# Performance work log

Measured on AMD Instinct MI355X. Metric: run time of the kernel, lower is better.

The kernel has to match this reference:

```python
import jax, jax.numpy as jnp
import numpy as np
from jax import lax
from jax.scipy.special import logsumexp

B, T, K, D = 16, 128, 1024, 768
APPROX_R = 0.1
LAMBD = 0.1
KP = int(APPROX_R * K)  # num_state_approx = 102


def setup_inputs() -> dict:
    key = jax.random.key(0)
    k0, k1, k2, k3 = jax.random.split(key, 4)
    x_emb = jax.random.normal(k0, (B, T, D), jnp.float32)
    # nn.Parameter(torch.normal(0, norm_scale_transition, [K, D]))
    state_matrix = 0.01 * jax.random.normal(k1, (K, D), jnp.float32)
    y = jax.random.randint(k2, (B, T), 0, K)
    y_lens = jax.random.randint(k3, (B,), 1, T + 1)
    return {"x_emb": x_emb, "state_matrix": state_matrix, "y": y, "y_lens": y_lens}


def _forward_sum(transition, emission, y_lens):
    # exact linear-chain CRF forward (logsumexp) scan. emission: [B,T,K]
    bsz = emission.shape[0]
    def step(alpha, em_t):
        new = logsumexp(alpha[:, :, None] + transition[None], axis=1) + em_t
        return new, new
    a0 = emission[:, 0]
    _, rest = lax.scan(step, a0, jnp.swapaxes(emission, 0, 1)[1:])
    alphas = jnp.concatenate([a0[None], rest], axis=0)  # [T,B,K]
    a_last = alphas[y_lens - 1, jnp.arange(bsz)]        # [B,K]
    return logsumexp(a_last, axis=-1)


def _approx_forward(state_matrix, emission, y_lens, kp):
    # restricted forward over the top-kp states (by emission potential) per
    # position; transitions among selected states computed on the fly from
    # state embeddings (avoids the full KxK transition).
    bsz = emission.shape[0]
    d = state_matrix.shape[1]
    em_top, idx = lax.top_k(emission, kp)   # [B,T,KP]
    st_sel = state_matrix[idx]              # [B,T,KP,D]
    def step(carry, inp):
        alpha, st_prev = carry
        em_t, st_t = inp
        trans_t = jnp.einsum('bid,bjd->bij', st_prev, st_t) / np.sqrt(d)
        new = logsumexp(alpha[:, :, None] + trans_t, axis=1) + em_t
        return (new, st_t), new
    a0 = em_top[:, 0]
    xs = (jnp.swapaxes(em_top, 0, 1)[1:], jnp.swapaxes(st_sel, 0, 1)[1:])
    _, rest = lax.scan(step, (a0, st_sel[:, 0]), xs)
    alphas = jnp.concatenate([a0[None], rest], axis=0)
    a_last = alphas[y_lens - 1, jnp.arange(bsz)]
    return logsumexp(a_last, axis=-1)


def _viterbi(transition, emission, y_lens):
    bsz, tlen, k = emission.shape
    def step(alpha, em_t):
        scores = alpha[:, :, None] + transition[None]
        bp = jnp.argmax(scores, axis=1).astype(jnp.int32)
        new = jnp.max(scores, axis=1) + em_t
        return new, (new, bp)
    a0 = emission[:, 0]
    _, (rest, bps) = lax.scan(step, a0, jnp.swapaxes(emission, 0, 1)[1:])
    alphas = jnp.concatenate([a0[None], rest], axis=0)  # [T,B,K]
    a_last = alphas[y_lens - 1, jnp.arange(bsz)]
    last_state = jnp.argmax(a_last, axis=-1).astype(jnp.int32)
    # bps[t] maps best state at t+1 -> state at t; pad to length T
    bps_pad = jnp.concatenate([bps, jnp.zeros((1, bsz, k), jnp.int32)], axis=0)
    def back(s, inp):
        t, bp_t = inp
        cand = jnp.take_along_axis(bp_t, s[:, None], axis=1)[:, 0]
        s_new = jnp.where(t == y_lens - 1, last_state,
                          jnp.where(t < y_lens - 1, cand, 0))
        return s_new, s_new
    ts = jnp.arange(tlen)[::-1]
    _, s_seq = lax.scan(back, jnp.zeros((bsz,), jnp.int32), (ts, bps_pad[::-1]))
    return jnp.swapaxes(s_seq[::-1], 0, 1)  # [B,T]


def _evaluate(y_pred, y, y_lens, mask_f):
    support = ((y > 0).astype(jnp.float32) * mask_f).sum()
    pred = ((y_pred > 0).astype(jnp.float32) * mask_f).sum()
    overlap = (((y_pred > 0) & (y > 0)).astype(jnp.float32) * mask_f).sum()
    acc = ((y_pred == y).astype(jnp.float32) * mask_f).sum() / y_lens.sum()
    prec = jnp.where(pred > 0, overlap / jnp.maximum(pred, 1.0), 0.0)
    recl = overlap / jnp.maximum(support, 1.0)
    f1 = jnp.where(prec > 0, 2 * prec * recl / jnp.maximum(prec + recl, 1e-12), 0.0)
    return acc, prec, recl, f1


def reference(x_emb, state_matrix, y, y_lens):
    d = x_emb.shape[-1]
    bsz, tlen = y.shape
    emission = jnp.einsum('btd,kd->btk', x_emb, state_matrix) / np.sqrt(d)
    transition = jnp.matmul(state_matrix, state_matrix.T) / np.sqrt(d)

    log_Z = _forward_sum(transition, emission, y_lens)
    log_Z_approx = _approx_forward(state_matrix, emission, y_lens, KP)

    # gold sequence log potential, masked by lengths
    pos = jnp.arange(tlen)
    mask = (pos[None, :] < y_lens[:, None])
    mask_f = mask.astype(jnp.float32)
    mask_tr = (pos[None, :tlen - 1] < (y_lens - 1)[:, None]).astype(jnp.float32)
    em_y = jnp.take_along_axis(emission, y[..., None], axis=-1)[..., 0]
    trans_y = transition[y[:, :-1], y[:, 1:]]
    log_y_potential = (em_y * mask_f).sum(-1) + (trans_y * mask_tr).sum(-1)

    seq_log_prob_exact = -(log_y_potential - log_Z).mean()
    seq_log_prob_approx = -(log_y_potential - log_Z_approx).mean()

    total_len = y_lens.sum()
    logp = jax.nn.log_softmax(emission, axis=-1)
    lp_y = jnp.take_along_axis(logp, y[..., None], axis=-1)[..., 0]
    seq_log_prob_local = (lp_y * mask_f).sum() / total_len
    max_prob = (jnp.max(jax.nn.softmax(emission, -1), -1) * mask_f).sum() / total_len

    # loss_type == 'approx_crf'
    loss = seq_log_prob_approx + LAMBD * seq_log_prob_local

    crf_output = _viterbi(transition, emission, y_lens)
    crf_acc, crf_prec, crf_recl, crf_f1 = _evaluate(crf_output, y, y_lens, mask_f)
    softmax_output = emission.argmax(-1)
    sm_acc, sm_prec, sm_recl, sm_f1 = _evaluate(softmax_output, y, y_lens, mask_f)

    return (loss, crf_output, log_Z.mean(), log_Z_approx.mean(),
            seq_log_prob_exact, seq_log_prob_local, max_prob,
            crf_acc, crf_f1, sm_acc, sm_f1)


if __name__ == '__main__':
    out = reference(**setup_inputs())
    print(out[0], out[2], out[3])
```

## Files before the change

kernel.cpp:

```cpp
#include <hip/hip_runtime.h>
#include <cstdint>
#include <cstddef>

typedef unsigned long long ull;
typedef unsigned int uint32;
typedef unsigned short u16;
typedef __attribute__((ext_vector_type(8))) short s8v;
typedef __attribute__((ext_vector_type(4))) float f32x4;


#define POISON32 0xFFFFFFFFu
#define POISON64 0xFFFFFFFFFFFFFFFFull

#define OFF_EM    ((size_t)0)
#define OFF_TR    ((size_t)2097152)
#define OFF_EXPTB ((size_t)3145728)
#define OFF_UPP   ((size_t)3670016)
#define OFF_APP   ((size_t)3735552)
#define OFF_ULST  ((size_t)3801088)
#define OFF_ALST  ((size_t)3817472)
#define OFF_UALST ((size_t)3833856)
#define OFF_ETOP  ((size_t)3835904)
#define OFF_ITOP  ((size_t)4044800)
#define OFF_RMAX  ((size_t)4253696)
#define OFF_RLSE  ((size_t)4255744)
#define OFF_SMP   ((size_t)4257792)
#define OFF_BP    ((size_t)4259840)
#define OFF_DONE  ((size_t)6356992)
#define OFF_EXPTT ((size_t)6367744)

__device__ __forceinline__ u16 f2bf(float f) {
  uint32 u = __builtin_bit_cast(uint32, f);
  u = (u + 0x7fffu + ((u >> 16) & 1u)) >> 16;
  return (u16)u;
}
__device__ __forceinline__ float bflo(uint32 w) {
  return __builtin_bit_cast(float, w << 16);
}
__device__ __forceinline__ float bfhi(uint32 w) {
  return __builtin_bit_cast(float, w & 0xffff0000u);
}
__device__ __forceinline__ void bfsplit(float v, u16& h, u16& l) {
  h = f2bf(v);
  float rh = __builtin_bit_cast(float, ((uint32)h) << 16);
  l = f2bf(v - rh);
}

__device__ __forceinline__ ull load_bypass_u64(const ull* p) {
  return __hip_atomic_load(p, __ATOMIC_RELAXED, __HIP_MEMORY_SCOPE_AGENT);
}
__device__ __forceinline__ void store_bypass_u64(ull* p, ull v) {
  __hip_atomic_store(p, v, __ATOMIC_RELAXED, __HIP_MEMORY_SCOPE_AGENT);
}
__device__ __forceinline__ uint32 load_bypass_u32(const uint32* p) {
  return __hip_atomic_load(p, __ATOMIC_RELAXED, __HIP_MEMORY_SCOPE_AGENT);
}
__device__ __forceinline__ void store_bypass_u32(uint32* p, uint32 v) {
  __hip_atomic_store(p, v, __ATOMIC_RELAXED, __HIP_MEMORY_SCOPE_AGENT);
}
__device__ __forceinline__ void store_bypass_u16(u16* p, u16 v) {
  __hip_atomic_store(p, v, __ATOMIC_RELAXED, __HIP_MEMORY_SCOPE_AGENT);
}
__device__ __forceinline__ float load_bypass_f(const float* p) {
  return __hip_atomic_load(p, __ATOMIC_RELAXED, __HIP_MEMORY_SCOPE_AGENT);
}
__device__ __forceinline__ void store_bypass_f(float* p, float v) {
  __hip_atomic_store(p, v, __ATOMIC_RELAXED, __HIP_MEMORY_SCOPE_AGENT);
}
__device__ __forceinline__ void store_bypass_i(int* p, int v) {
  __hip_atomic_store(p, v, __ATOMIC_RELAXED, __HIP_MEMORY_SCOPE_AGENT);
}
__device__ __forceinline__ int load_bypass_i(const int* p) {
  return __hip_atomic_load(p, __ATOMIC_RELAXED, __HIP_MEMORY_SCOPE_AGENT);
}

__global__ __launch_bounds__(256) void gemm_kernel(
    const float* __restrict__ x, const float* __restrict__ stm,
    float* __restrict__ emission, float* __restrict__ transition,
    u16* __restrict__ expTb) {
  __shared__ float As[16][68];
  __shared__ float Bs[16][68];
  const int tid = threadIdx.x;
  const int tx = tid & 15, ty = tid >> 4;
  const int m0 = blockIdx.x * 64, n0 = blockIdx.y * 64;
  const int lr = tid >> 2;
  const int lc = (tid & 3) << 2;
  float acc[4][4] = {};
  const float* aptr;
  {
    int gr = m0 + lr;
    aptr = (gr < 2048) ? (x + (size_t)gr * 768) : (stm + (size_t)(gr - 2048) * 768);
  }
  const float* bptr = stm + (size_t)(n0 + lr) * 768;
  for (int k0 = 0; k0 < 768; k0 += 16) {
    float4 a4 = *(const float4*)(aptr + k0 + lc);
    float4 b4 = *(const float4*)(bptr + k0 + lc);
    __syncthreads();
    As[lc + 0][lr] = a4.x; As[lc + 1][lr] = a4.y; As[lc + 2][lr] = a4.z; As[lc + 3][lr] = a4.w;
    Bs[lc + 0][lr] = b4.x; Bs[lc + 1][lr] = b4.y; Bs[lc + 2][lr] = b4.z; Bs[lc + 3][lr] = b4.w;
    __syncthreads();
#pragma unroll
    for (int kk = 0; kk < 16; ++kk) {
      float a[4], b[4];
#pragma unroll
      for (int q = 0; q < 4; ++q) a[q] = As[kk][ty * 4 + q];
#pragma unroll
      for (int q = 0; q < 4; ++q) b[q] = Bs[kk][tx * 4 + q];
#pragma unroll
      for (int i2 = 0; i2 < 4; ++i2)
#pragma unroll
        for (int j2 = 0; j2 < 4; ++j2) acc[i2][j2] += a[i2] * b[j2];
    }
  }
  const float rs = 0.03608439182435161f;
#pragma unroll
  for (int i2 = 0; i2 < 4; ++i2) {
    int r = m0 + ty * 4 + i2;
#pragma unroll
    for (int j2 = 0; j2 < 4; ++j2) {
      int c = n0 + tx * 4 + j2;
      float v = acc[i2][j2] * rs;
      if (r < 2048) {
        emission[(size_t)r * 1024 + c] = v;
      } else {
        size_t o = (size_t)(r - 2048) * 1024 + c;
        transition[o] = v;
        expTb[o] = f2bf(expf(v));
      }
    }
  }
}

__global__ __launch_bounds__(256) void transT_kernel(
    const u16* __restrict__ src, u16* __restrict__ dst) {
  __shared__ u16 tile[64][65];
  const int bx = blockIdx.x * 64, by = blockIdx.y * 64;
  const int tx = threadIdx.x & 63, ty4 = threadIdx.x >> 6;
  for (int rr = ty4; rr < 64; rr += 4)
    tile[rr][tx] = src[(size_t)(bx + rr) * 1024 + by + tx];
  __syncthreads();
  for (int rr = ty4; rr < 64; rr += 4)
    dst[(size_t)(by + rr) * 1024 + bx + tx] = tile[tx][rr];
}

__global__ __launch_bounds__(256) void topk_kernel(
    const float* __restrict__ emission, float* __restrict__ em_top,
    int* __restrict__ top_idx, float* __restrict__ row_max,
    float* __restrict__ row_lse, int* __restrict__ sm_pred) {
  __shared__ float v[1024];
  __shared__ int ix[1024];
  __shared__ float rb[256];
  const int row = blockIdx.x;
  const int tid = threadIdx.x;
  const float* e = emission + (size_t)row * 1024;
  for (int p = tid; p < 1024; p += 256) { v[p] = e[p]; ix[p] = p; }
  __syncthreads();
  for (int k = 2; k <= 1024; k <<= 1) {
    for (int j = k >> 1; j > 0; j >>= 1) {
      for (int p = tid; p < 1024; p += 256) {
        int l = p ^ j;
        if (l > p) {
          float va = v[p], vb = v[l];
          int ia = ix[p], ib = ix[l];
          bool aBefore = (va > vb) || (va == vb && ia < ib);
          bool up = ((p & k) == 0);
          if (up ? !aBefore : aBefore) { v[p] = vb; v[l] = va; ix[p] = ib; ix[l] = ia; }
        }
      }
      __syncthreads();
    }
  }
  float mx = v[0];
  float s = 0.f;
  for (int p = tid; p < 1024; p += 256) s += expf(v[p] - mx);
  rb[tid] = s; __syncthreads();
  for (int w = 128; w > 0; w >>= 1) { if (tid < w) rb[tid] += rb[tid + w]; __syncthreads(); }
  if (tid == 0) {
    row_max[row] = mx;
    row_lse[row] = mx + logf(rb[0]);
    sm_pred[row] = ix[0];
  }
  for (int p = tid; p < 102; p += 256) {
    em_top[(size_t)row * 102 + p] = v[p];
    top_idx[(size_t)row * 102 + p] = ix[p];
  }
}

__global__ __launch_bounds__(256) void poison_kernel(ull* __restrict__ done8) {
  const int idx = blockIdx.x * 256 + threadIdx.x;
  store_bypass_u64(done8 + idx, POISON64);
}

__global__ __launch_bounds__(512) void scan_kernel(
    const float* __restrict__ em, const float* __restrict__ tr,
    const u16* __restrict__ expTb, const u16* __restrict__ expTbT,
    const float* __restrict__ em_top, const int* __restrict__ top_idx,
    const int* __restrict__ y_lens,
    float* __restrict__ u_ring, float* __restrict__ av_ring,
    float* __restrict__ u_last, float* __restrict__ av_last,
    float* __restrict__ ua_last, int* __restrict__ bp,
    uint32* __restrict__ done, float* __restrict__ out_crf) {
  __shared__ ull SH[9232];
  const int bid = blockIdx.x, tid = threadIdx.x;
  uint32* sentF = done;
  uint32* sentV = done + 512;
  uint32* vdone = done + 8704;

  if (bid < 8) {
    const int p = bid;
    int* stbF = (int*)(SH + 8192);
    if (tid < 16) stbF[tid] = y_lens[tid] - 1;
    const int l = tid & 63;
    const int lm = l & 15, lq = l >> 4;
    const int w2 = (tid >> 6) & 3;
    if (tid < 256) {
      const int m = tid >> 4;
      const int nn = p * 128 + ((tid & 15) << 3);
      const float* e0 = em + ((size_t)m << 17) + nn;
      u16* rh = (u16*)u_ring;
      const bool last0 = (y_lens[m] == 1);
#pragma unroll
      for (int q = 0; q < 8; ++q) {
        float v = expf(e0[q]);
        u16 h, lo2; bfsplit(v, h, lo2);
        store_bypass_u16(rh + m * 1024 + nn + q, h);
        store_bypass_u16(rh + 16384 + m * 1024 + nn + q, lo2);
        if (last0) u_last[(size_t)m * 1024 + nn + q] = v;
      }
    }
    __syncthreads();
    if (tid == 0) {
      asm volatile("s_waitcnt vmcnt(0)" ::: "memory");
      store_bypass_u32(sentF + p * 16, 0u);
    }
    const char* Ab = (const char*)SH;
    const int offh = (lm << 11) + (lq << 4);
    const int axor = (lm & 7) << 4;
    const int nbase = p * 128 + w2 * 32;
    const u16* bq0 = expTbT + ((size_t)(nbase + lm) << 10) + (lq << 3);
    const u16* bq1 = bq0 + (16 << 10);
    for (int t = 1; t < 128; ++t) {
      if (tid < 8) {
        const uint32* sp = sentF + (size_t)((t - 1) & 3) * 128 + tid * 16;
        while (load_bypass_u32(sp) == POISON32) __builtin_amdgcn_s_sleep(1);
      }
      __syncthreads();
      if (tid == 0)
        store_bypass_u32(sentF + (size_t)((t + 2) & 3) * 128 + p * 16, POISON32);
      {
        const ull* src = (const ull*)(u_ring + (size_t)((t - 1) & 3) * 16384);
        ull dbuf[16];
#pragma unroll
        for (int q = 0; q < 16; ++q) dbuf[q] = load_bypass_u64(src + tid + (q << 9));
#pragma unroll
        for (int q = 0; q < 16; ++q) {
          const int ob = (tid + (q << 9)) << 3;
          *(ull*)((char*)SH + (ob ^ (((ob >> 11) & 7) << 4))) = dbuf[q];
        }
      }
      __syncthreads();
      if (tid < 256) {
        f32x4 acc0a = {0.f, 0.f, 0.f, 0.f}, acc0b = {0.f, 0.f, 0.f, 0.f};
        f32x4 acc1a = {0.f, 0.f, 0.f, 0.f}, acc1b = {0.f, 0.f, 0.f, 0.f};
        for (int k0 = 0; k0 < 1024; k0 += 64) {
          const int o0 = (offh + (k0 << 1)) ^ axor;
          const int o1 = (offh + ((k0 + 32) << 1)) ^ axor;
          s8v ah0 = *(const s8v*)(Ab + o0);
          s8v al0 = *(const s8v*)(Ab + 32768 + o0);
          s8v ah1 = *(const s8v*)(Ab + o1);
          s8v al1 = *(const s8v*)(Ab + 32768 + o1);
          s8v b00 = *(const s8v*)(bq0 + k0);
          s8v b10 = *(const s8v*)(bq1 + k0);
          s8v b01 = *(const s8v*)(bq0 + k0 + 32);
          s8v b11 = *(const s8v*)(bq1 + k0 + 32);
          acc0a = __builtin_amdgcn_mfma_f32_16x16x32_bf16(ah0, b00, acc0a, 0, 0, 0);
          acc1a = __builtin_amdgcn_mfma_f32_16x16x32_bf16(ah0, b10, acc1a, 0, 0, 0);
          acc0b = __builtin_amdgcn_mfma_f32_16x16x32_bf16(ah1, b01, acc0b, 0, 0, 0);
          acc1b = __builtin_amdgcn_mfma_f32_16x16x32_bf16(ah1, b11, acc1b, 0, 0, 0);
          acc0a = __builtin_amdgcn_mfma_f32_16x16x32_bf16(al0, b00, acc0a, 0, 0, 0);
          acc1a = __builtin_amdgcn_mfma_f32_16x16x32_bf16(al0, b10, acc1a, 0, 0, 0);
          acc0b = __builtin_amdgcn_mfma_f32_16x16x32_bf16(al1, b01, acc0b, 0, 0, 0);
          acc1b = __builtin_amdgcn_mfma_f32_16x16x32_bf16(al1, b11, acc1b, 0, 0, 0);
        }
        u16* rh = (u16*)(u_ring + (size_t)(t & 3) * 16384);
        const float sc = 1.0f / 1024.0f;
#pragma unroll
        for (int r = 0; r < 4; ++r) {
          const int m = (lq << 2) + r;
          const size_t erow = (((size_t)m << 7) + t) << 10;
          {
            const int n = nbase + lm;
            float v = (acc0a[r] + acc0b[r]) * sc * expf(em[erow + n]);
            u16 h, lo2; bfsplit(v, h, lo2);
            store_bypass_u16(rh + m * 1024 + n, h);
            store_bypass_u16(rh + 16384 + m * 1024 + n, lo2);
            if (t == stbF[m]) u_last[(size_t)m * 1024 + n] = v;
          }
          {
            const int n = nbase + 16 + lm;
            float v = (acc1a[r] + acc1b[r]) * sc * expf(em[erow + n]);
            u16 h, lo2; bfsplit(v, h, lo2);
            store_bypass_u16(rh + m * 1024 + n, h);
            store_bypass_u16(rh + 16384 + m * 1024 + n, lo2);
            if (t == stbF[m]) u_last[(size_t)m * 1024 + n] = v;
          }
        }
        asm volatile("s_waitcnt vmcnt(0)" ::: "memory");
      }
      __syncthreads();
      if (tid == 0) store_bypass_u32(sentF + (size_t)(t & 3) * 128 + p * 16, 0u);
    }
  } else if (bid < 136) {
    const int v = bid - 8;
    const int n0v = ((v & 7) << 7) + ((v >> 3) << 3);
    const int jj = tid & 7, g = tid >> 3;
    const int col = n0v + jj;
    ull* ppb = (ull*)((char*)SH + 65536);
    int* stb2 = (int*)((char*)SH + 73728);
    if (tid < 16) stb2[tid] = y_lens[tid] - 1;
    if (tid < 128) {
      const int jb = tid & 7, b = tid >> 3;
      const float e0 = em[((size_t)b << 17) + n0v + jb];
      store_bypass_f(av_ring + (size_t)(n0v + jb) * 16 + b, e0);
      if (y_lens[b] == 1) store_bypass_f(av_last + ((size_t)b << 10) + n0v + jb, e0);
    }
    __syncthreads();
    if (tid == 0) {
      asm volatile("s_waitcnt vmcnt(0)" ::: "memory");
      store_bypass_u32(sentV + v * 16, 0u);
    }
    const char* stc = (const char*)SH;
    for (int t = 1; t < 128; ++t) {
      if (tid < 128) {
        const uint32* sp = sentV + (size_t)((t - 1) & 3) * 2048 + tid * 16;
        while (load_bypass_u32(sp) == POISON32) __builtin_amdgcn_s_sleep(1);
      }
      __syncthreads();
      if (tid == 0)
        store_bypass_u32(sentV + (size_t)((t + 2) & 3) * 2048 + v * 16, POISON32);
      {
        const ull* src = (const ull*)(av_ring + (size_t)((t - 1) & 3) * 16384);
        ull dbuf[16];
#pragma unroll
        for (int q = 0; q < 16; ++q) dbuf[q] = load_bypass_u64(src + tid + (q << 9));
#pragma unroll
        for (int q = 0; q < 16; ++q) {
          const int ob = (tid + (q << 9)) << 3;
          *(ull*)((char*)SH + (ob ^ (((ob >> 10) & 7) << 4))) = dbuf[q];
        }
      }
      __syncthreads();
      float mv[16]; int mi[16];
#pragma unroll
      for (int b = 0; b < 16; ++b) { mv[b] = -3.0e38f; mi[b] = 0x7fffffff; }
      const float* trc = tr + col;
      const int i0 = g << 4;
#pragma unroll 4
      for (int ii = 0; ii < 16; ++ii) {
        const int i = i0 + ii;
        const float tv = trc[(size_t)i << 10];
        const int ph = (i << 6) ^ (((i >> 4) & 7) << 4);
        const f32x4 s0 = *(const f32x4*)(stc + (ph ^ 0));
        const f32x4 s1 = *(const f32x4*)(stc + (ph ^ 16));
        const f32x4 s2 = *(const f32x4*)(stc + (ph ^ 32));
        const f32x4 s3 = *(const f32x4*)(stc + (ph ^ 48));
#pragma unroll
        for (int b = 0; b < 4; ++b) {
          float c0 = s0[b] + tv; if (c0 > mv[b])      { mv[b] = c0;      mi[b] = i; }
          float c1 = s1[b] + tv; if (c1 > mv[b + 4])  { mv[b + 4] = c1;  mi[b + 4] = i; }
          float c2 = s2[b] + tv; if (c2 > mv[b + 8])  { mv[b + 8] = c2;  mi[b + 8] = i; }
          float c3 = s3[b] + tv; if (c3 > mv[b + 12]) { mv[b + 12] = c3; mi[b + 12] = i; }
        }
      }
#pragma unroll
      for (int d = 8; d <= 32; d <<= 1) {
#pragma unroll
        for (int b = 0; b < 16; ++b) {
          float ov = __shfl_xor(mv[b], d);
          int oi = __shfl_xor(mi[b], d);
          if (ov > mv[b] || (ov == mv[b] && oi < mi[b])) { mv[b] = ov; mi[b] = oi; }
        }
      }
      if ((tid & 63) < 8) {
        const int wv = tid >> 6;
#pragma unroll
        for (int b = 0; b < 16; ++b) {
          ull pk = ((ull)(uint32)mi[b] << 32) | (ull)__builtin_bit_cast(uint32, mv[b]);
          ppb[(b << 6) + (wv << 3) + jj] = pk;
        }
      }
      __syncthreads();
      if (tid < 128) {
        const int jb = tid & 7, b = tid >> 3;
        const int cf = n0v + jb;
        float bmv = -3.0e38f; int bmi = 0x7fffffff;
#pragma unroll
        for (int w = 0; w < 8; ++w) {
          ull pk = ppb[(b << 6) + (w << 3) + jb];
          float pv = __builtin_bit_cast(float, (uint32)pk);
          int pi = (int)(pk >> 32);
          if (pv > bmv || (pv == bmv && pi < bmi)) { bmv = pv; bmi = pi; }
        }
        const float nv = bmv + em[((((size_t)b << 7) + t) << 10) + cf];
        store_bypass_f(av_ring + (size_t)(t & 3) * 16384 + (size_t)cf * 16 + b, nv);
        store_bypass_i(bp + ((size_t)t << 14) + ((size_t)b << 10) + cf, bmi);
        if (t == stb2[b]) store_bypass_f(av_last + ((size_t)b << 10) + cf, nv);
        asm volatile("s_waitcnt vmcnt(0)" ::: "memory");
      }
      __syncthreads();
      if (tid == 0) store_bypass_u32(sentV + (size_t)(t & 3) * 2048 + v * 16, 0u);
    }
    if (tid == 0) {
      asm volatile("s_waitcnt vmcnt(0)" ::: "memory");
      store_bypass_u32(vdone + v * 16, 0u);
    }
    if (v == 0) {
      if (tid < 128) {
        while (load_bypass_u32(vdone + tid * 16) == POISON32) __builtin_amdgcn_s_sleep(1);
      }
      __syncthreads();
      const int wv = tid >> 6, lh = tid & 63;
      const int hb = lh >> 5, hl = lh & 31;
      const int b = wv * 2 + hb;
      const int tbb = y_lens[b] - 1;
      for (int t2 = tbb + 1 + hl; t2 < 128; t2 += 32) out_crf[(b << 7) + t2] = 0.f;
      float bv = -3.0e38f; int bi = 0x7fffffff;
      for (int q = 0; q < 32; ++q) {
        const int i = (q << 5) + hl;
        const float val = load_bypass_f(av_last + ((size_t)b << 10) + i);
        if (val > bv || (val == bv && i < bi)) { bv = val; bi = i; }
      }
#pragma unroll
      for (int d = 1; d < 32; d <<= 1) {
        float ov = __shfl_xor(bv, d, 32);
        int oi = __shfl_xor(bi, d, 32);
        if (ov > bv || (ov == bv && oi < bi)) { bv = ov; bi = oi; }
      }
      if (hl == 0) {
        int sx = bi;
        out_crf[(b << 7) + tbb] = (float)sx;
        for (int t2 = tbb - 1; t2 >= 0; --t2) {
          sx = load_bypass_i(bp + ((size_t)(t2 + 1) << 14) + ((size_t)b << 10) + sx);
          out_crf[(b << 7) + t2] = (float)sx;
        }
      }
    }
  } else {
    const int b = bid - 136;
    const int tb = y_lens[b] - 1;
    const int j2 = tid & 127, h2 = tid >> 7;
    float* sua0 = (float*)SH;
    float* sua1 = sua0 + 104;
    int* sidxp = (int*)(sua0 + 208);
    int* sidxc = sidxp + 104;
    float* aps = (float*)(sidxc + 104);
    if (tid < 102) {
      float vv = expf(em_top[(size_t)(b * 128) * 102 + tid]);
      sua0[tid] = vv;
      if (tb == 0) ua_last[b * 102 + tid] = vv;
    }
    __syncthreads();
    for (int t = 1; t < 128; ++t) {
      if (tid < 102) sidxp[tid] = top_idx[((size_t)b * 128 + (t - 1)) * 102 + tid];
      else if (tid >= 256 && tid < 358)
        sidxc[tid - 256] = top_idx[((size_t)b * 128 + t) * 102 + (tid - 256)];
      __syncthreads();
      float acc2 = 0.f;
      float* up = (t & 1) ? sua0 : sua1;
      float* cur = (t & 1) ? sua1 : sua0;
      if (j2 < 102) {
        const int colc = sidxc[j2];
        const int ia = h2 * 26;
        const int ib2 = (ia + 26 < 102) ? ia + 26 : 102;
        for (int i = ia; i < ib2; ++i)
          acc2 += up[i] * bflo((uint32)expTb[(size_t)sidxp[i] * 1024 + colc]);
      }
      if (h2 > 0 && j2 < 102) aps[(h2 - 1) * 104 + j2] = acc2;
      __syncthreads();
      if (h2 == 0 && j2 < 102) {
        acc2 += aps[j2] + aps[104 + j2] + aps[208 + j2];
        const float e = em_top[((size_t)b * 128 + t) * 102 + j2];
        const float nv = acc2 * expf(e) * (1.0f / 102.0f);
        cur[j2] = nv;
        if (t == tb) ua_last[b * 102 + j2] = nv;
      }
      __syncthreads();
    }
  }
}

__device__ __forceinline__ float blk_sum(float v, float* rb, int tid) {
  rb[tid] = v; __syncthreads();
  for (int w = 128; w > 0; w >>= 1) { if (tid < w) rb[tid] += rb[tid + w]; __syncthreads(); }
  float r = rb[0]; __syncthreads();
  return r;
}

__global__ __launch_bounds__(256) void finalize_kernel(
    const float* __restrict__ emission, const float* __restrict__ transition,
    const float* __restrict__ u_last, const float* __restrict__ ua_last,
    const float* __restrict__ row_max, const float* __restrict__ row_lse,
    const int* __restrict__ sm_pred, const int* __restrict__ y,
    const int* __restrict__ y_lens, float* __restrict__ d_out) {
  __shared__ float rb[256];
  __shared__ float sZ[16], sZa[16], sLogy[16];
  const int tid = threadIdx.x;
  const float* out_crf = d_out + 1;
  for (int b = 0; b < 16; ++b) {
    const int tb = y_lens[b] - 1;
    float p = 0.f;
    for (int i = tid; i < 1024; i += 256) p += u_last[(size_t)b * 1024 + i];
    p = blk_sum(p, rb, tid);
    if (tid == 0) sZ[b] = logf(p) + (float)tb * 6.931471805599453f;
    float q = 0.f;
    for (int i = tid; i < 102; i += 256) q += ua_last[(size_t)b * 102 + i];
    q = blk_sum(q, rb, tid);
    if (tid == 0) sZa[b] = logf(q) + (float)tb * 4.624972813284271f;
  }
  if (tid < 16) sLogy[tid] = 0.f;
  __syncthreads();
  float a_local = 0, a_maxp = 0, c_sup = 0, c_pred = 0, c_ov = 0, c_match = 0;
  float s_predc = 0, s_ov = 0, s_match = 0;
  for (int r = tid; r < 2048; r += 256) {
    const int b = r >> 7, t = r & 127;
    const int L = y_lens[b];
    if (t < L) {
      const int yv = y[r];
      const float em_y = emission[(size_t)r * 1024 + yv];
      const float lse = row_lse[r];
      a_local += em_y - lse;
      a_maxp += expf(row_max[r] - lse);
      float term = em_y;
      if (t < L - 1) term += transition[(size_t)yv * 1024 + y[r + 1]];
      atomicAdd(&sLogy[b], term);
      const float ypos = (yv > 0) ? 1.f : 0.f;
      c_sup += ypos;
      const int cs = (int)out_crf[r];
      c_pred += (cs > 0) ? 1.f : 0.f;
      c_ov += ((cs > 0) && (yv > 0)) ? 1.f : 0.f;
      c_match += (cs == yv) ? 1.f : 0.f;
      const int ss = sm_pred[r];
      s_predc += (ss > 0) ? 1.f : 0.f;
      s_ov += ((ss > 0) && (yv > 0)) ? 1.f : 0.f;
      s_match += (ss == yv) ? 1.f : 0.f;
    }
  }
  __syncthreads();
  a_local = blk_sum(a_local, rb, tid);
  a_maxp = blk_sum(a_maxp, rb, tid);
  c_sup = blk_sum(c_sup, rb, tid);
  c_pred = blk_sum(c_pred, rb, tid);
  c_ov = blk_sum(c_ov, rb, tid);
  c_match = blk_sum(c_match, rb, tid);
  s_predc = blk_sum(s_predc, rb, tid);
  s_ov = blk_sum(s_ov, rb, tid);
  s_match = blk_sum(s_match, rb, tid);
  if (tid == 0) {
    float tl = 0.f;
    for (int b = 0; b < 16; ++b) tl += (float)y_lens[b];
    float mZ = 0, mZa = 0, dE = 0, dA = 0;
    for (int b = 0; b < 16; ++b) {
      mZ += sZ[b]; mZa += sZa[b];
      dE += sLogy[b] - sZ[b];
      dA += sLogy[b] - sZa[b];
    }
    mZ *= (1.f / 16.f); mZa *= (1.f / 16.f);
    const float sle = -dE * (1.f / 16.f);
    const float sla = -dA * (1.f / 16.f);
    const float slocal = a_local / tl;
    const float maxp = a_maxp / tl;
    const float loss = sla + 0.1f * slocal;
    const float crf_acc = c_match / tl;
    const float crf_prec = (c_pred > 0.f) ? (c_ov / fmaxf(c_pred, 1.f)) : 0.f;
    const float crf_recl = c_ov / fmaxf(c_sup, 1.f);
    const float crf_f1 = (crf_prec > 0.f)
        ? (2.f * crf_prec * crf_recl / fmaxf(crf_prec + crf_recl, 1e-12f)) : 0.f;
    const float sm_acc = s_match / tl;
    const float sm_prec = (s_predc > 0.f) ? (s_ov / fmaxf(s_predc, 1.f)) : 0.f;
    const float sm_recl = s_ov / fmaxf(c_sup, 1.f);
    const float sm_f1 = (sm_prec > 0.f)
        ? (2.f * sm_prec * sm_recl / fmaxf(sm_prec + sm_recl, 1e-12f)) : 0.f;
    d_out[0] = loss;
    d_out[2049] = mZ;
    d_out[2050] = mZa;
    d_out[2051] = sle;
    d_out[2052] = slocal;
    d_out[2053] = maxp;
    d_out[2054] = crf_acc;
    d_out[2055] = crf_f1;
    d_out[2056] = sm_acc;
    d_out[2057] = sm_f1;
  }
}

extern "C" void kernel_launch(void* const* d_in, const int* in_sizes, int n_in,
                              void* d_out, int out_size, void* d_ws, size_t ws_size,
                              hipStream_t stream) {
  const float* x = (const float*)d_in[0];
  const float* stm = (const float*)d_in[1];
  const int* y = (const int*)d_in[2];
  const int* yl = (const int*)d_in[3];
  float* out = (float*)d_out;
  float* ws = (float*)d_ws;

  float* emission = ws + OFF_EM;
  float* transition = ws + OFF_TR;
  u16* expTb = (u16*)(ws + OFF_EXPTB);
  u16* expTbT = (u16*)(ws + OFF_EXPTT);
  float* u_ring = ws + OFF_UPP;
  float* av_ring = ws + OFF_APP;
  float* u_last = ws + OFF_ULST;
  float* av_last = ws + OFF_ALST;
  float* ua_last = ws + OFF_UALST;
  float* em_top = ws + OFF_ETOP;
  int* top_idx = (int*)(ws + OFF_ITOP);
  float* row_max = ws + OFF_RMAX;
  float* row_lse = ws + OFF_RLSE;
  int* sm_pred = (int*)(ws + OFF_SMP);
  int* bp = (int*)(ws + OFF_BP);
  uint32* done = (uint32*)(ws + OFF_DONE);

  poison_kernel<<<21, 256, 0, stream>>>((ull*)done);
  gemm_kernel<<<dim3(48, 16), 256, 0, stream>>>(x, stm, emission, transition, expTb);
  transT_kernel<<<dim3(16, 16), 256, 0, stream>>>(expTb, expTbT);
  topk_kernel<<<2048, 256, 0, stream>>>(emission, em_top, top_idx, row_max, row_lse, sm_pred);
  scan_kernel<<<152, 512, 0, stream>>>(emission, transition, expTb, expTbT, em_top, top_idx,
                                       yl, u_ring, av_ring, u_last, av_last, ua_last,
                                       bp, done, out + 1);
  finalize_kernel<<<1, 256, 0, stream>>>(emission, transition, u_last, ua_last,
                                         row_max, row_lse, sm_pred, y, yl, out);
}
```

Measured before the change: 1.914 ms.

## Replace per-block poison flags with atomic arrival counters in scan sync

Swaps the cross-block handshake in the persistent scan kernel. Each producer block used to write its own flag, and consumers polled many flags and re-poisoned slots in a 4-deep ring. Now producer blocks atomically increment a shared counter per ring slot (one counter per slot for the 8 forward blocks, and per slot and column group for the 128 Viterbi blocks), and a few threads poll it against a monotonically increasing target. The aim is to cut per-step polling traffic and the re-poison stores, at the cost of atomic contention on a handful of counters. The vmcnt wait moves to every writing thread before the barrier.

```diff
diff --git a/kernel.cpp b/kernel.cpp
--- a/kernel.cpp
+++ b/kernel.cpp
@@ -8,9 +8,6 @@
 typedef __attribute__((ext_vector_type(8))) short s8v;
 typedef __attribute__((ext_vector_type(4))) float f32x4;
 
-
-#define POISON32 0xFFFFFFFFu
-#define POISON64 0xFFFFFFFFFFFFFFFFull
 
 #define OFF_EM    ((size_t)0)
 #define OFF_TR    ((size_t)2097152)
@@ -72,6 +69,9 @@
 }
 __device__ __forceinline__ int load_bypass_i(const int* p) {
   return __hip_atomic_load(p, __ATOMIC_RELAXED, __HIP_MEMORY_SCOPE_AGENT);
+}
+__device__ __forceinline__ void cnt_add(uint32* p) {
+  __hip_atomic_fetch_add(p, 1u, __ATOMIC_RELAXED, __HIP_MEMORY_SCOPE_AGENT);
 }
 
 __global__ __launch_bounds__(256) void gemm_kernel(
@@ -186,9 +186,9 @@
   }
 }
 
-__global__ __launch_bounds__(256) void poison_kernel(ull* __restrict__ done8) {
+__global__ __launch_bounds__(256) void zero_kernel(uint32* __restrict__ done) {
   const int idx = blockIdx.x * 256 + threadIdx.x;
-  store_bypass_u64(done8 + idx, POISON64);
+  store_bypass_u32(done + idx, 0u);
 }
 
 __global__ __launch_bounds__(512) void scan_kernel(
@@ -202,9 +202,9 @@
     uint32* __restrict__ done, float* __restrict__ out_crf) {
   __shared__ ull SH[9232];
   const int bid = blockIdx.x, tid = threadIdx.x;
-  uint32* sentF = done;
-  uint32* sentV = done + 512;
-  uint32* vdone = done + 8704;
+  uint32* cntF = done;
+  uint32* cntV = done + 64;
+  uint32* vdone = done + 640;
 
   if (bid < 8) {
     const int p = bid;
@@ -227,12 +227,10 @@
         store_bypass_u16(rh + 16384 + m * 1024 + nn + q, lo2);
         if (last0) u_last[(size_t)m * 1024 + nn + q] = v;
       }
+      asm volatile("s_waitcnt vmcnt(0)" ::: "memory");
     }
     __syncthreads();
-    if (tid == 0) {
-      asm volatile("s_waitcnt vmcnt(0)" ::: "memory");
-      store_bypass_u32(sentF + p * 16, 0u);
-    }
+    if (tid == 0) cnt_add(cntF + 0);
     const char* Ab = (const char*)SH;
     const int offh = (lm << 11) + (lq << 4);
     const int axor = (lm & 7) << 4;
@@ -240,13 +238,12 @@
     const u16* bq0 = expTbT + ((size_t)(nbase + lm) << 10) + (lq << 3);
     const u16* bq1 = bq0 + (16 << 10);
     for (int t = 1; t < 128; ++t) {
-      if (tid < 8) {
-        const uint32* sp = sentF + (size_t)((t - 1) & 3) * 128 + tid * 16;
-        while (load_bypass_u32(sp) == POISON32) __builtin_amdgcn_s_sleep(1);
-      }
-      __syncthreads();
-      if (tid == 0)
-        store_bypass_u32(sentF + (size_t)((t + 2) & 3) * 128 + p * 16, POISON32);
+      if (tid == 0) {
+        const uint32 tgt = (uint32)((((t - 1) >> 2) + 1) * 8);
+        const uint32* cp = cntF + (((t - 1) & 3) << 4);
+        while (load_bypass_u32(cp) < tgt) __builtin_amdgcn_s_sleep(1);
+      }
+      __syncthreads();
       {
         const ull* src = (const ull*)(u_ring + (size_t)((t - 1) & 3) * 16384);
         ull dbuf[16];
@@ -308,7 +305,7 @@
         asm volatile("s_waitcnt vmcnt(0)" ::: "memory");
       }
       __syncthreads();
-      if (tid == 0) store_bypass_u32(sentF + (size_t)(t & 3) * 128 + p * 16, 0u);
+      if (tid == 0) cnt_add(cntF + ((t & 3) << 4));
     }
   } else if (bid < 136) {
     const int v = bid - 8;
@@ -323,21 +320,18 @@
       const float e0 = em[((size_t)b << 17) + n0v + jb];
       store_bypass_f(av_ring + (size_t)(n0v + jb) * 16 + b, e0);
       if (y_lens[b] == 1) store_bypass_f(av_last + ((size_t)b << 10) + n0v + jb, e0);
+      asm volatile("s_waitcnt vmcnt(0)" ::: "memory");
     }
     __syncthreads();
-    if (tid == 0) {
-      asm volatile("s_waitcnt vmcnt(0)" ::: "memory");
-      store_bypass_u32(sentV + v * 16, 0u);
-    }
+    if (tid == 0) cnt_add(cntV + ((v & 7) << 4));
     const char* stc = (const char*)SH;
     for (int t = 1; t < 128; ++t) {
-      if (tid < 128) {
-        const uint32* sp = sentV + (size_t)((t - 1) & 3) * 2048 + tid * 16;
-        while (load_bypass_u32(sp) == POISON32) __builtin_amdgcn_s_sleep(1);
-      }
-      __syncthreads();
-      if (tid == 0)
-        store_bypass_u32(sentV + (size_t)((t + 2) & 3) * 2048 + v * 16, POISON32);
+      if (tid < 8) {
+        const uint32 tgt = (uint32)((((t - 1) >> 2) + 1) * 16);
+        const uint32* cp = cntV + (((((t - 1) & 3) << 3) + tid) << 4);
+        while (load_bypass_u32(cp) < tgt) __builtin_amdgcn_s_sleep(1);
+      }
+      __syncthreads();
       {
         const ull* src = (const ull*)(av_ring + (size_t)((t - 1) & 3) * 16384);
         ull dbuf[16];
@@ -408,15 +402,12 @@
         asm volatile("s_waitcnt vmcnt(0)" ::: "memory");
       }
       __syncthreads();
-      if (tid == 0) store_bypass_u32(sentV + (size_t)(t & 3) * 2048 + v * 16, 0u);
-    }
-    if (tid == 0) {
-      asm volatile("s_waitcnt vmcnt(0)" ::: "memory");
-      store_bypass_u32(vdone + v * 16, 0u);
-    }
+      if (tid == 0) cnt_add(cntV + ((((t & 3) << 3) + (v & 7)) << 4));
+    }
+    if (tid == 0) cnt_add(vdone);
     if (v == 0) {
-      if (tid < 128) {
-        while (load_bypass_u32(vdone + tid * 16) == POISON32) __builtin_amdgcn_s_sleep(1);
+      if (tid == 0) {
+        while (load_bypass_u32(vdone) < 128u) __builtin_amdgcn_s_sleep(1);
       }
       __syncthreads();
       const int wv = tid >> 6, lh = tid & 63;
@@ -620,7 +611,7 @@
   int* bp = (int*)(ws + OFF_BP);
   uint32* done = (uint32*)(ws + OFF_DONE);
 
-  poison_kernel<<<21, 256, 0, stream>>>((ull*)done);
+  zero_kernel<<<4, 256, 0, stream>>>(done);
   gemm_kernel<<<dim3(48, 16), 256, 0, stream>>>(x, stm, emission, transition, expTb);
   transT_kernel<<<dim3(16, 16), 256, 0, stream>>>(expTb, expTbT);
   topk_kernel<<<2048, 256, 0, stream>>>(emission, em_top, top_idx, row_max, row_lse, sm_pred);
```

Result: no change. 1.902 ms (-0.6%).
